# Optimization experiments

Hardware: AMD Instinct MI355X
Metric: run time of the kernel (lower is better)

Reference implementation:

```python
import jax, jax.numpy as jnp
import numpy as np

NB, T, NS, NC = 1024, 128, 12, 4
N = NS + NC  # stacked state+control dim


def setup_inputs() -> dict:
    key = jax.random.key(0)
    ks = jax.random.split(key, 7)
    x_init = jax.random.normal(ks[0], (NB, NS), jnp.float32)
    current_x = jax.random.normal(ks[1], (NB, T, NS), jnp.float32)
    current_u = jax.random.normal(ks[2], (NB, T, NC), jnp.float32)
    # symmetric positive-definite cost Hessian per (batch, t)
    G = 0.1 * jax.random.normal(ks[3], (NB, T, N, N), jnp.float32)
    Q = 0.5 * (G + jnp.swapaxes(G, -1, -2)) + jnp.eye(N, dtype=jnp.float32)
    p = jax.random.normal(ks[4], (NB, T, N), jnp.float32)
    # stable per-step dynamics linearizations
    A = 0.95 * jnp.eye(NS, dtype=jnp.float32) + 0.02 * jax.random.normal(ks[5], (NB, T, NS, NS), jnp.float32)
    Bmat = 0.1 * jax.random.normal(ks[6], (NB, T, NS, NC), jnp.float32)
    time = jnp.arange(T, dtype=jnp.int32)
    return {"x_init": x_init, "current_x": current_x, "current_u": current_u,
            "Q": Q, "p": p, "A": A, "Bmat": Bmat, "time": time}


def _lqr_backward(Q, p, A, Bmat):
    # time-major for scan: (T, NB, ...)
    Qs = jnp.moveaxis(Q, 1, 0)
    ps = jnp.moveaxis(p, 1, 0)
    As = jnp.moveaxis(A, 1, 0)
    Bs = jnp.moveaxis(Bmat, 1, 0)
    nb = Q.shape[0]
    V0 = jnp.zeros((nb, NS, NS), Q.dtype)  # V=0 reproduces the t==T-1 branch
    v0 = jnp.zeros((nb, NS), Q.dtype)

    def step(carry, inp):
        V, v = carry
        Qt0, pt, At, Bt = inp
        F = jnp.concatenate([At, Bt], axis=-1)          # (nb, ns, n)
        FT = jnp.swapaxes(F, -1, -2)                    # (nb, n, ns)
        Qt = Qt0 + FT @ V @ F                           # (nb, n, n)
        qt = pt + jnp.einsum('bsn,bs->bn', F, v)        # F^T v
        Qxx, Qxu = Qt[..., :NS, :NS], Qt[..., :NS, NS:]
        Qux, Quu = Qt[..., NS:, :NS], Qt[..., NS:, NS:]
        qx, qu = qt[..., :NS], qt[..., NS:]
        Quu_inv = jnp.linalg.pinv(Quu)                  # (nb, nc, nc)
        Kt = -(Quu_inv @ Qux)                           # (nb, nc, ns)
        kt = -jnp.einsum('bij,bj->bi', Quu_inv, qu)     # (nb, nc)
        KtT = jnp.swapaxes(Kt, -1, -2)
        Vn = Qxx + Qxu @ Kt + KtT @ Qux + KtT @ Quu @ Kt
        vn = (qx + jnp.einsum('bij,bj->bi', Qxu, kt)
              + jnp.einsum('bij,bj->bi', KtT, qu)
              + jnp.einsum('bij,bj->bi', KtT @ Quu, kt))
        return (Vn, vn), (Kt, kt)

    _, (K, k) = jax.lax.scan(step, (V0, v0), (Qs, ps, As, Bs), reverse=True)
    return jnp.moveaxis(K, 0, 1), jnp.moveaxis(k, 0, 1)


def _lqr_forward(x_init, current_u, Q, p, A, Bmat, K, k):
    Ks = jnp.moveaxis(K, 1, 0)
    ks_ = jnp.moveaxis(k, 1, 0)
    As = jnp.moveaxis(A, 1, 0)
    Bs = jnp.moveaxis(Bmat, 1, 0)
    cus = jnp.moveaxis(current_u, 1, 0)
    Qs = jnp.moveaxis(Q, 1, 0)
    ps = jnp.moveaxis(p, 1, 0)
    nb = x_init.shape[0]
    cost0 = jnp.zeros((nb,), x_init.dtype)

    def step(carry, inp):
        xt, cost = carry
        Kt, kt, At, Bt, cut, Qt, pt = inp
        # NOTE: original module never updates delta_x (stays zero), so delta_u == k_t
        ut = cut + kt
        xut = jnp.concatenate([xt, ut], axis=-1)        # (nb, n)
        xnext = jnp.einsum('bij,bj->bi', At, xt) + jnp.einsum('bij,bj->bi', Bt, ut)
        cost = cost + 0.5 * jnp.einsum('bi,bij,bj->b', xut, Qt, xut) + jnp.sum(xut * pt, axis=-1)
        return (xnext, cost), (xt, ut)

    (_, cost), (xs, us) = jax.lax.scan(step, (x_init, cost0), (Ks, ks_, As, Bs, cus, Qs, ps))
    # xs holds x_0..x_{T-1}, matching return of x[..., 0:-1, :]
    return jnp.moveaxis(xs, 0, 1), jnp.moveaxis(us, 0, 1), cost


def reference(x_init, current_x, current_u, Q, p, A, Bmat, time):
    K, k = _lqr_backward(Q, p, A, Bmat)
    return _lqr_forward(x_init, current_u, Q, p, A, Bmat, K, k)
```

## Files before the change

kernel.cpp:

```cpp
#include <hip/hip_runtime.h>


#define NBQ 1024
#define TT  128

__device__ __forceinline__ float dotf4(float4 a, float4 b) {
  return a.x*b.x + a.y*b.y + a.z*b.z + a.w*b.w;
}
__device__ __forceinline__ float dpp_qx1(float x) {
  return __int_as_float(__builtin_amdgcn_mov_dpp(__float_as_int(x), 0xB1, 0xF, 0xF, true));
}
__device__ __forceinline__ float dpp_qx2(float x) {
  return __int_as_float(__builtin_amdgcn_mov_dpp(__float_as_int(x), 0x4E, 0xF, 0xF, true));
}
template<int Q> __device__ __forceinline__ float4 bcast4(float4 v) {
  float4 r;
  r.x = __int_as_float(__builtin_amdgcn_mov_dpp(__float_as_int(v.x), Q*0x55, 0xF, 0xF, true));
  r.y = __int_as_float(__builtin_amdgcn_mov_dpp(__float_as_int(v.y), Q*0x55, 0xF, 0xF, true));
  r.z = __int_as_float(__builtin_amdgcn_mov_dpp(__float_as_int(v.z), Q*0x55, 0xF, 0xF, true));
  r.w = __int_as_float(__builtin_amdgcn_mov_dpp(__float_as_int(v.w), Q*0x55, 0xF, 0xF, true));
  return r;
}

#define MKS(K, O, MY)  { float4 mk_ = bcast4<O>(MY);                           \
  qt4_.x += gk_[K]*mk_.x; qt4_.y += gk_[K]*mk_.y;                              \
  qt4_.z += gk_[K]*mk_.z; qt4_.w += gk_[K]*mk_.w; }

#define BW_BODY(T_, QV, PV, CV, P0,P1,P2, S0,S1,S2, FTC, FTN)                  \
{                                                                              \
  const int  t_   = (T_);                                                      \
  const long bt_  = b*TT + t_;                                                 \
  const long btL_ = b*TT + ((t_ >= 4) ? (t_ - 4) : 0);                         \
  float4 qN_ = *(const float4*)(Qg + btL_*256 + qoff);                         \
  const float* fpL_ = fBase + btL_*fMul + fOfs;                                \
  float fN0_ = fpL_[0], fN1_ = fpL_[fstr_], fN2_ = fpL_[2*fstr_];              \
  float  pN_ = pg[btL_*16 + j];                                                \
  float  cN_ = cug[btL_*4 + q4];                                               \
             \
  FTN[wix] = P0; FTN[wix+1] = P1; FTN[wix+2] = P2;                             \
   \
  const float4* fj4_ = (const float4*)(FTC + j*12);                            \
  float4 f0_=fj4_[0], f1_=fj4_[1], f2_=fj4_[2];                                \
  const float4* vrow_ = (const float4*)(Vs + (3*r + dmin)*12);                 \
  float4 mv0_=vrow_[0], mv1_=vrow_[1], mv2_=vrow_[2];                          \
  float4 mw_ = *(const float4*)(vvS + 4*dmin);                                 \
   \
  float m0_, m1_, m2_;                                                         \
  { float4 r0_=bcast4<0>(mv0_), r1_=bcast4<0>(mv1_), r2_=bcast4<0>(mv2_);      \
    m0_ = dotf4(r0_,f0_)+dotf4(r1_,f1_)+dotf4(r2_,f2_); }                      \
  { float4 r0_=bcast4<1>(mv0_), r1_=bcast4<1>(mv1_), r2_=bcast4<1>(mv2_);      \
    m1_ = dotf4(r0_,f0_)+dotf4(r1_,f1_)+dotf4(r2_,f2_); }                      \
  { float4 r0_=bcast4<2>(mv0_), r1_=bcast4<2>(mv1_), r2_=bcast4<2>(mv2_);      \
    m2_ = dotf4(r0_,f0_)+dotf4(r1_,f1_)+dotf4(r2_,f2_); }                      \
  msh[(3*r+0)*16 + j] = m0_;                                                   \
  msh[(3*r+1)*16 + j] = m1_;                                                   \
  msh[(3*r+2)*16 + j] = m2_;                                                   \
                \
  float qtv_;                                                                  \
  { float4 w0_=bcast4<0>(mw_), w1_=bcast4<1>(mw_), w2_=bcast4<2>(mw_);         \
    qtv_ = PV + dotf4(w0_,f0_)+dotf4(w1_,f1_)+dotf4(w2_,f2_); }                \
                    \
  float gk_[12] = {f0_.x,f0_.y,f0_.z,f0_.w, f1_.x,f1_.y,f1_.z,f1_.w,           \
                   f2_.x,f2_.y,f2_.z,f2_.w};                                   \
  float4 mys0_ = *(const float4*)(msh + (3*q4+0)*16 + cb4);                    \
  float4 mys1_ = *(const float4*)(msh + (3*q4+1)*16 + cb4);                    \
  float4 mys2_ = *(const float4*)(msh + (3*q4+2)*16 + cb4);                    \
  float4 qt4_ = QV;                                                            \
  MKS(0,0,mys0_) MKS(1,0,mys1_) MKS(2,0,mys2_)                                 \
  MKS(3,1,mys0_) MKS(4,1,mys1_) MKS(5,1,mys2_)                                 \
  MKS(6,2,mys0_) MKS(7,2,mys1_) MKS(8,2,mys2_)                                 \
  MKS(9,3,mys0_) MKS(10,3,mys1_) MKS(11,3,mys2_)                               \
                                            \
  if (j >= 12)           *(float4*)(UxS + (j-12)*16 + cb4) = qt4_;             \
  if (cb == 3 && j < 12) *(float4*)(XuS + j*4) = qt4_;                         \
  if (l >= 12 && l < 16) quS[l-12] = qtv_;                                     \
   \
   \
  float4 mmA_ = *(const float4*)(UxS + 0*16 + 12);                             \
  float4 mmB_ = *(const float4*)(UxS + 1*16 + 12);                             \
  float4 mmC_ = *(const float4*)(UxS + 2*16 + 12);                             \
  float4 mmD_ = *(const float4*)(UxS + 3*16 + 12);                             \
  float4 ux0_ = *(const float4*)(UxS + 0*16 + cb4);                            \
  float4 ux1_ = *(const float4*)(UxS + 1*16 + cb4);                            \
  float4 ux2_ = *(const float4*)(UxS + 2*16 + cb4);                            \
  float4 ux3_ = *(const float4*)(UxS + 3*16 + cb4);                            \
  float4 quv_   = *(const float4*)quS;                                         \
  float4 xr_    = *(const float4*)(XuS + jc*4);                                \
  float mm_[16] = { mmA_.x, mmA_.y, mmA_.z, mmA_.w,                            \
                    mmB_.x, mmB_.y, mmB_.z, mmB_.w,                            \
                    mmC_.x, mmC_.y, mmC_.z, mmC_.w,                            \
                    mmD_.x, mmD_.y, mmD_.z, mmD_.w };                          \
    \
  float rdp_ = __builtin_amdgcn_rcpf(mm_[0]*mm_[5] - mm_[1]*mm_[1]);           \
  float pi00_ = mm_[5]*rdp_, pi01_ = -mm_[1]*rdp_, pi11_ = mm_[0]*rdp_;        \
  float w00_ = pi00_*mm_[2] + pi01_*mm_[6];                                    \
  float w01_ = pi00_*mm_[3] + pi01_*mm_[7];                                    \
  float w10_ = pi01_*mm_[2] + pi11_*mm_[6];                                    \
  float w11_ = pi01_*mm_[3] + pi11_*mm_[7];                                    \
  float t00_ = mm_[10] - (mm_[2]*w00_ + mm_[6]*w10_);                          \
  float t01_ = mm_[11] - (mm_[2]*w01_ + mm_[6]*w11_);                          \
  float t11_ = mm_[15] - (mm_[3]*w01_ + mm_[7]*w11_);                          \
  float rdt_ = __builtin_amdgcn_rcpf(t00_*t11_ - t01_*t01_);                   \
  float ti00_ = t11_*rdt_, ti01_ = -t01_*rdt_, ti11_ = t00_*rdt_;              \
  float u00_ = -(w00_*ti00_ + w01_*ti01_);                                     \
  float u01_ = -(w00_*ti01_ + w01_*ti11_);                                     \
  float u10_ = -(w10_*ti00_ + w11_*ti01_);                                     \
  float u11_ = -(w10_*ti01_ + w11_*ti11_);                                     \
  float i00_ = pi00_ - (u00_*w00_ + u01_*w01_);                                \
  float i01_ = pi01_ - (u00_*w10_ + u01_*w11_);                                \
  float i11_ = pi11_ - (u10_*w10_ + u11_*w11_);                                \
  float inv_[16] = { i00_, i01_, u00_, u01_,                                   \
                     i01_, i11_, u10_, u11_,                                   \
                     u00_, u10_, ti00_, ti01_,                                 \
                     u01_, u11_, ti01_, ti11_ };                               \
  float kt0_ = -(inv_[0] *quv_.x + inv_[1] *quv_.y + inv_[2] *quv_.z + inv_[3] *quv_.w); \
  float kt1_ = -(inv_[4] *quv_.x + inv_[5] *quv_.y + inv_[6] *quv_.z + inv_[7] *quv_.w); \
  float kt2_ = -(inv_[8] *quv_.x + inv_[9] *quv_.y + inv_[10]*quv_.z + inv_[11]*quv_.w); \
  float kt3_ = -(inv_[12]*quv_.x + inv_[13]*quv_.y + inv_[14]*quv_.z + inv_[15]*quv_.w); \
  float4 kc_[4];                                                               \
  _Pragma("unroll")                                                            \
  for (int c_ = 0; c_ < 4; ++c_) {                                             \
    kc_[c_].x = -(inv_[c_*4+0]*ux0_.x + inv_[c_*4+1]*ux1_.x + inv_[c_*4+2]*ux2_.x + inv_[c_*4+3]*ux3_.x); \
    kc_[c_].y = -(inv_[c_*4+0]*ux0_.y + inv_[c_*4+1]*ux1_.y + inv_[c_*4+2]*ux2_.y + inv_[c_*4+3]*ux3_.y); \
    kc_[c_].z = -(inv_[c_*4+0]*ux0_.z + inv_[c_*4+1]*ux1_.z + inv_[c_*4+2]*ux2_.z + inv_[c_*4+3]*ux3_.z); \
    kc_[c_].w = -(inv_[c_*4+0]*ux0_.w + inv_[c_*4+1]*ux1_.w + inv_[c_*4+2]*ux2_.w + inv_[c_*4+3]*ux3_.w); \
  }                                                                            \
  if (j < 12) {                                                                \
    float4 vn4_;                                                               \
    vn4_.x = qt4_.x + xr_.x*kc_[0].x + xr_.y*kc_[1].x + xr_.z*kc_[2].x + xr_.w*kc_[3].x; \
    vn4_.y = qt4_.y + xr_.x*kc_[0].y + xr_.y*kc_[1].y + xr_.z*kc_[2].y + xr_.w*kc_[3].y; \
    vn4_.z = qt4_.z + xr_.x*kc_[0].z + xr_.y*kc_[1].z + xr_.z*kc_[2].z + xr_.w*kc_[3].z; \
    vn4_.w = qt4_.w + xr_.x*kc_[0].w + xr_.y*kc_[1].w + xr_.z*kc_[2].w + xr_.w*kc_[3].w; \
    if (cb < 3) *(float4*)(Vs + j*12 + cb4) = vn4_;                            \
  }                                                                            \
  if (l < 12)                                                                  \
    vvS[l] = qtv_ + xr_.x*kt0_ + xr_.y*kt1_ + xr_.z*kt2_ + xr_.w*kt3_;         \
  float uv_ = CV + ((q4==0)?kt0_:(q4==1)?kt1_:(q4==2)?kt2_:kt3_);              \
  if (l < 4) { us_out[bt_*4 + l] = uv_; uL[t_*4 + l] = uv_; }                  \
  QV = qN_; S0 = fN0_; S1 = fN1_; S2 = fN2_; PV = pN_; CV = cN_;               \
}

__global__ __launch_bounds__(64, 1) void lqr_fused(
    const float* __restrict__ Qg, const float* __restrict__ pg,
    const float* __restrict__ Ag, const float* __restrict__ Bg,
    const float* __restrict__ cug, const float* __restrict__ xinit,
    float* __restrict__ out)
{
  __shared__ __align__(16) float lds[1376];
  float* FT0 = lds;
  float* FT1 = lds + 192;
  float* Vs  = lds + 384;
  float* vvS = lds + 528;
  float* msh = lds + 544;
  float* UxS = lds + 736;
  float* XuS = lds + 800;
  float* quS = lds + 848;
  float* uL  = lds + 864;

  const int l    = threadIdx.x;
  const int j    = l & 15;
  const int r    = l >> 4;
  const int q4   = l & 3;
  const int cb   = l >> 4;
  const int cb4  = cb << 2;
  const int dmin = (q4 < 2) ? q4 : 2;
  const int jc   = (j < 12) ? j : 11;
  const long b   = blockIdx.x;

  const int  n_   = l >> 2;
  const int  k0_  = 3*(l & 3);
  const int  wix  = n_*12 + k0_;
  const bool isA  = (n_ < 12);
  const float* fBase = isA ? Ag : Bg;
  const int  fMul  = isA ? 144 : 48;
  const int  fstr_ = isA ? 12  : 4;
  const int  fOfs  = isA ? (k0_*12 + n_) : (k0_*4 + (n_ - 12));
  const int  qoff  = j * 16 + cb4;

  float* xs_out = out;
  float* us_out = out + (long)NBQ*TT*12;
  float* c_out  = out + (long)NBQ*TT*12 + (long)NBQ*TT*4;

  if (j < 12 && cb < 3) *(float4*)(Vs + j*12 + cb4) = make_float4(0.f,0.f,0.f,0.f);
  if (l < 12) vvS[l] = 0.f;

  const long base = b*TT;
  float4 q3v,q2v,q1v,q0v;
  float  p3v,c3v,p2v,c2v,p1v,c1v,p0v,c0v;
  float  f3a,f3b,f3c, f2a,f2b,f2c, f1a,f1b,f1c, f0a,f0b,f0c;
  {
    long bt;
    bt = base+127; q3v=*(const float4*)(Qg+bt*256+qoff); p3v=pg[bt*16+j]; c3v=cug[bt*4+q4];
    { const float* fp = fBase + bt*fMul + fOfs; f3a=fp[0]; f3b=fp[fstr_]; f3c=fp[2*fstr_]; }
    bt = base+126; q2v=*(const float4*)(Qg+bt*256+qoff); p2v=pg[bt*16+j]; c2v=cug[bt*4+q4];
    { const float* fp = fBase + bt*fMul + fOfs; f2a=fp[0]; f2b=fp[fstr_]; f2c=fp[2*fstr_]; }
    bt = base+125; q1v=*(const float4*)(Qg+bt*256+qoff); p1v=pg[bt*16+j]; c1v=cug[bt*4+q4];
    { const float* fp = fBase + bt*fMul + fOfs; f1a=fp[0]; f1b=fp[fstr_]; f1c=fp[2*fstr_]; }
    bt = base+124; q0v=*(const float4*)(Qg+bt*256+qoff); p0v=pg[bt*16+j]; c0v=cug[bt*4+q4];
    { const float* fp = fBase + bt*fMul + fOfs; f0a=fp[0]; f0b=fp[fstr_]; f0c=fp[2*fstr_]; }
  }
  FT1[wix] = f3a; FT1[wix+1] = f3b; FT1[wix+2] = f3c;

  #pragma unroll 1
  for (int tb = TT-1; tb >= 3; tb -= 4) {
    BW_BODY(tb,   q3v, p3v, c3v,  f2a,f2b,f2c,  f3a,f3b,f3c, FT1, FT0)
    BW_BODY(tb-1, q2v, p2v, c2v,  f1a,f1b,f1c,  f2a,f2b,f2c, FT0, FT1)
    BW_BODY(tb-2, q1v, p1v, c1v,  f0a,f0b,f0c,  f1a,f1b,f1c, FT1, FT0)
    BW_BODY(tb-3, q0v, p0v, c0v,  f3a,f3b,f3c,  f0a,f0b,f0c, FT0, FT1)
  }

  const int i4  = l >> 2;
  const int c0f = q4 << 2;
  const int i4c = (i4 < 12) ? i4 : 11;
  const int sl0 = (c0f+0)<<2, sl1 = (c0f+1)<<2, sl2 = (c0f+2)<<2, sl3 = (c0f+3)<<2;
  float s = xinit[b*12 + i4c];
  float cacc = 0.f;

  const long bt0 = base;
  float4 qfA = *(const float4*)(Qg + bt0*256 + 4*l);
  float4 ffA = (q4 < 3) ? *(const float4*)(Ag + bt0*144 + i4c*12 + c0f)
                        : *(const float4*)(Bg + bt0*48  + i4c*4);
  float  pfA = pg[bt0*16 + i4];
  float4 qfB = *(const float4*)(Qg + (bt0+1)*256 + 4*l);
  float4 ffB = (q4 < 3) ? *(const float4*)(Ag + (bt0+1)*144 + i4c*12 + c0f)
                        : *(const float4*)(Bg + (bt0+1)*48  + i4c*4);
  float  pfB = pg[(bt0+1)*16 + i4];
  float4 qfC = *(const float4*)(Qg + (bt0+2)*256 + 4*l);
  float4 ffC = (q4 < 3) ? *(const float4*)(Ag + (bt0+2)*144 + i4c*12 + c0f)
                        : *(const float4*)(Bg + (bt0+2)*48  + i4c*4);
  float  pfC = pg[(bt0+2)*16 + i4];

  #pragma unroll 1
  for (int t = 0; t < TT; ++t) {
    const long btp = bt0 + ((t+3 < TT-1) ? t+3 : TT-1);
    float4 qfD = *(const float4*)(Qg + btp*256 + 4*l);
    float4 ffD = (q4 < 3) ? *(const float4*)(Ag + btp*144 + i4c*12 + c0f)
                          : *(const float4*)(Bg + btp*48  + i4c*4);
    float  pfD = pg[btp*16 + i4];

    float4 u4 = *(const float4*)(uL + t*4);

    float4 xg;
    xg.x = __shfl(s, sl0, 64); xg.y = __shfl(s, sl1, 64);
    xg.z = __shfl(s, sl2, 64); xg.w = __shfl(s, sl3, 64);
    float4 xuq = (q4 < 3) ? xg : u4;
    float xui = (i4 < 12) ? s
              : (i4 == 12) ? u4.x : (i4 == 13) ? u4.y : (i4 == 14) ? u4.z : u4.w;

    if (q4 == 0 && i4 < 12) xs_out[(bt0+t)*12 + i4] = s;

    cacc += 0.5f * xui * dotf4(qfA, xuq);
    if (q4 == 0) cacc += xui * pfA;

    float zx = dotf4(ffA, xuq);
    zx += dpp_qx1(zx);
    zx += dpp_qx2(zx);
    s = zx;

    qfA = qfB; ffA = ffB; pfA = pfB;
    qfB = qfC; ffB = ffC; pfB = pfC;
    qfC = qfD; ffC = ffD; pfC = pfD;
  }

  cacc += __shfl_xor(cacc, 32, 64);
  cacc += __shfl_xor(cacc, 16, 64);
  cacc += __shfl_xor(cacc, 8, 64);
  cacc += __shfl_xor(cacc, 4, 64);
  cacc += dpp_qx2(cacc);
  cacc += dpp_qx1(cacc);
  if (l == 0) c_out[b] = cacc;
}

extern "C" void kernel_launch(void* const* d_in, const int* in_sizes, int n_in,
                              void* d_out, int out_size, void* d_ws, size_t ws_size,
                              hipStream_t stream) {
  const float* xinit = (const float*)d_in[0];
  const float* cu = (const float*)d_in[2];
  const float* Q  = (const float*)d_in[3];
  const float* p  = (const float*)d_in[4];
  const float* A  = (const float*)d_in[5];
  const float* Bm = (const float*)d_in[6];
  float* out = (float*)d_out;

  lqr_fused<<<dim3(NBQ), dim3(64), 0, stream>>>(Q, p, A, Bm, cu, xinit, out);
}
```

Baseline: 381.8 us.

## Buffer per-step outputs in LDS, swizzle staging, and remove divergent branches

The per-timestep global stores of us and xs are now written into LDS buffers and flushed with coalesced 64-wide stores after each loop. The Qt staging area is unified into a swizzled float4 array, and the V/v state is stored per lane so stores need no branches. Divergent conditionals are replaced with dummy-slot pointer writes and a multiplicative mask. This aims to cut scattered global stores, LDS bank conflicts and branch overhead on the serial critical path, at the cost of more LDS per block.

```diff
diff --git a/kernel.cpp b/kernel.cpp
--- a/kernel.cpp
+++ b/kernel.cpp
@@ -3,6 +3,8 @@
 
 #define NBQ 1024
 #define TT  128
+
+#define SSLOT(x) ((x) ^ ((((x) >> 4) << 1)))
 
 __device__ __forceinline__ float dotf4(float4 a, float4 b) {
   return a.x*b.x + a.y*b.y + a.z*b.z + a.w*b.w;
@@ -29,7 +31,6 @@
 #define BW_BODY(T_, QV, PV, CV, P0,P1,P2, S0,S1,S2, FTC, FTN)                  \
 {                                                                              \
   const int  t_   = (T_);                                                      \
-  const long bt_  = b*TT + t_;                                                 \
   const long btL_ = b*TT + ((t_ >= 4) ? (t_ - 4) : 0);                         \
   float4 qN_ = *(const float4*)(Qg + btL_*256 + qoff);                         \
   const float* fpL_ = fBase + btL_*fMul + fOfs;                                \
@@ -38,12 +39,11 @@
   float  cN_ = cug[btL_*4 + q4];                                               \
              \
   FTN[wix] = P0; FTN[wix+1] = P1; FTN[wix+2] = P2;                             \
-   \
+          \
   const float4* fj4_ = (const float4*)(FTC + j*12);                            \
   float4 f0_=fj4_[0], f1_=fj4_[1], f2_=fj4_[2];                                \
-  const float4* vrow_ = (const float4*)(Vs + (3*r + dmin)*12);                 \
-  float4 mv0_=vrow_[0], mv1_=vrow_[1], mv2_=vrow_[2];                          \
-  float4 mw_ = *(const float4*)(vvS + 4*dmin);                                 \
+  float4 mv0_ = vns4[kR], mv1_ = vns4[16+kR], mv2_ = vns4[32+kR];              \
+  float4 mw_ = *(const float4*)(vvF + 4*dmin);                                 \
    \
   float m0_, m1_, m2_;                                                         \
   { float4 r0_=bcast4<0>(mv0_), r1_=bcast4<0>(mv1_), r2_=bcast4<0>(mv2_);      \
@@ -55,10 +55,11 @@
   msh[(3*r+0)*16 + j] = m0_;                                                   \
   msh[(3*r+1)*16 + j] = m1_;                                                   \
   msh[(3*r+2)*16 + j] = m2_;                                                   \
-                \
+   \
   float qtv_;                                                                  \
   { float4 w0_=bcast4<0>(mw_), w1_=bcast4<1>(mw_), w2_=bcast4<2>(mw_);         \
     qtv_ = PV + dotf4(w0_,f0_)+dotf4(w1_,f1_)+dotf4(w2_,f2_); }                \
+  qtS[l] = qtv_;                                                               \
                     \
   float gk_[12] = {f0_.x,f0_.y,f0_.z,f0_.w, f1_.x,f1_.y,f1_.z,f1_.w,           \
                    f2_.x,f2_.y,f2_.z,f2_.w};                                   \
@@ -70,27 +71,21 @@
   MKS(3,1,mys0_) MKS(4,1,mys1_) MKS(5,1,mys2_)                                 \
   MKS(6,2,mys0_) MKS(7,2,mys1_) MKS(8,2,mys2_)                                 \
   MKS(9,3,mys0_) MKS(10,3,mys1_) MKS(11,3,mys2_)                               \
-                                            \
-  if (j >= 12)           *(float4*)(UxS + (j-12)*16 + cb4) = qt4_;             \
-  if (cb == 3 && j < 12) *(float4*)(XuS + j*4) = qt4_;                         \
-  if (l >= 12 && l < 16) quS[l-12] = qtv_;                                     \
+              \
+  stg4[sw_] = qt4_;                                                            \
    \
-   \
-  float4 mmA_ = *(const float4*)(UxS + 0*16 + 12);                             \
-  float4 mmB_ = *(const float4*)(UxS + 1*16 + 12);                             \
-  float4 mmC_ = *(const float4*)(UxS + 2*16 + 12);                             \
-  float4 mmD_ = *(const float4*)(UxS + 3*16 + 12);                             \
-  float4 ux0_ = *(const float4*)(UxS + 0*16 + cb4);                            \
-  float4 ux1_ = *(const float4*)(UxS + 1*16 + cb4);                            \
-  float4 ux2_ = *(const float4*)(UxS + 2*16 + cb4);                            \
-  float4 ux3_ = *(const float4*)(UxS + 3*16 + cb4);                            \
-  float4 quv_   = *(const float4*)quS;                                         \
-  float4 xr_    = *(const float4*)(XuS + jc*4);                                \
+  float4 mmA_ = stg4[SSLOT(60)];                                               \
+  float4 mmB_ = stg4[SSLOT(61)];                                               \
+  float4 mmC_ = stg4[SSLOT(62)];                                               \
+  float4 mmD_ = stg4[SSLOT(63)];                                               \
+  float4 ux0_ = stg4[sux0], ux1_ = stg4[sux1], ux2_ = stg4[sux2], ux3_ = stg4[sux3]; \
+  float4 quv_ = *(const float4*)(qtS + 12);                                    \
+  float4 xr_  = stg4[sxr];                                                     \
   float mm_[16] = { mmA_.x, mmA_.y, mmA_.z, mmA_.w,                            \
                     mmB_.x, mmB_.y, mmB_.z, mmB_.w,                            \
                     mmC_.x, mmC_.y, mmC_.z, mmC_.w,                            \
                     mmD_.x, mmD_.y, mmD_.z, mmD_.w };                          \
-    \
+                           \
   float rdp_ = __builtin_amdgcn_rcpf(mm_[0]*mm_[5] - mm_[1]*mm_[1]);           \
   float pi00_ = mm_[5]*rdp_, pi01_ = -mm_[1]*rdp_, pi11_ = mm_[0]*rdp_;        \
   float w00_ = pi00_*mm_[2] + pi01_*mm_[6];                                    \
@@ -125,18 +120,16 @@
     kc_[c_].z = -(inv_[c_*4+0]*ux0_.z + inv_[c_*4+1]*ux1_.z + inv_[c_*4+2]*ux2_.z + inv_[c_*4+3]*ux3_.z); \
     kc_[c_].w = -(inv_[c_*4+0]*ux0_.w + inv_[c_*4+1]*ux1_.w + inv_[c_*4+2]*ux2_.w + inv_[c_*4+3]*ux3_.w); \
   }                                                                            \
-  if (j < 12) {                                                                \
-    float4 vn4_;                                                               \
-    vn4_.x = qt4_.x + xr_.x*kc_[0].x + xr_.y*kc_[1].x + xr_.z*kc_[2].x + xr_.w*kc_[3].x; \
-    vn4_.y = qt4_.y + xr_.x*kc_[0].y + xr_.y*kc_[1].y + xr_.z*kc_[2].y + xr_.w*kc_[3].y; \
-    vn4_.z = qt4_.z + xr_.x*kc_[0].z + xr_.y*kc_[1].z + xr_.z*kc_[2].z + xr_.w*kc_[3].z; \
-    vn4_.w = qt4_.w + xr_.x*kc_[0].w + xr_.y*kc_[1].w + xr_.z*kc_[2].w + xr_.w*kc_[3].w; \
-    if (cb < 3) *(float4*)(Vs + j*12 + cb4) = vn4_;                            \
-  }                                                                            \
-  if (l < 12)                                                                  \
-    vvS[l] = qtv_ + xr_.x*kt0_ + xr_.y*kt1_ + xr_.z*kt2_ + xr_.w*kt3_;         \
+                           \
+  float4 vn4_;                                                                 \
+  vn4_.x = qt4_.x + xr_.x*kc_[0].x + xr_.y*kc_[1].x + xr_.z*kc_[2].x + xr_.w*kc_[3].x; \
+  vn4_.y = qt4_.y + xr_.x*kc_[0].y + xr_.y*kc_[1].y + xr_.z*kc_[2].y + xr_.w*kc_[3].y; \
+  vn4_.z = qt4_.z + xr_.x*kc_[0].z + xr_.y*kc_[1].z + xr_.z*kc_[2].z + xr_.w*kc_[3].z; \
+  vn4_.w = qt4_.w + xr_.x*kc_[0].w + xr_.y*kc_[1].w + xr_.z*kc_[2].w + xr_.w*kc_[3].w; \
+  vns4[l] = vn4_;                                                              \
+  vvF[l] = qtv_ + xr_.x*kt0_ + xr_.y*kt1_ + xr_.z*kt2_ + xr_.w*kt3_;           \
   float uv_ = CV + ((q4==0)?kt0_:(q4==1)?kt1_:(q4==2)?kt2_:kt3_);              \
-  if (l < 4) { us_out[bt_*4 + l] = uv_; uL[t_*4 + l] = uv_; }                  \
+  upt[0] = uv_; upt -= ustp;                                                   \
   QV = qN_; S0 = fN0_; S1 = fN1_; S2 = fN2_; PV = pN_; CV = cN_;               \
 }
 
@@ -146,16 +139,17 @@
     const float* __restrict__ cug, const float* __restrict__ xinit,
     float* __restrict__ out)
 {
-  __shared__ __align__(16) float lds[1376];
-  float* FT0 = lds;
-  float* FT1 = lds + 192;
-  float* Vs  = lds + 384;
-  float* vvS = lds + 528;
-  float* msh = lds + 544;
-  float* UxS = lds + 736;
-  float* XuS = lds + 800;
-  float* quS = lds + 848;
-  float* uL  = lds + 864;
+  __shared__ __align__(16) float lds[3328];
+  float*  FT0  = lds;
+  float*  FT1  = lds + 192;
+  float*  msh  = lds + 384;
+  float4* stg4 = (float4*)(lds + 576);
+  float4* vns4 = (float4*)(lds + 832);
+  float*  qtS  = lds + 1088;
+  float*  vvF  = lds + 1152;
+  float*  uL   = lds + 1216;
+  float*  dmpS = lds + 1728;
+  float*  xsL  = lds + 1792;
 
   const int l    = threadIdx.x;
   const int j    = l & 15;
@@ -166,6 +160,12 @@
   const int dmin = (q4 < 2) ? q4 : 2;
   const int jc   = (j < 12) ? j : 11;
   const long b   = blockIdx.x;
+  const int  kR  = 3*r + dmin;
+
+  const int sw_  = SSLOT(l);
+  const int sux0 = SSLOT(16*cb + 12), sux1 = SSLOT(16*cb + 13);
+  const int sux2 = SSLOT(16*cb + 14), sux3 = SSLOT(16*cb + 15);
+  const int sxr  = SSLOT(48 + jc);
 
   const int  n_   = l >> 2;
   const int  k0_  = 3*(l & 3);
@@ -177,12 +177,16 @@
   const int  fOfs  = isA ? (k0_*12 + n_) : (k0_*4 + (n_ - 12));
   const int  qoff  = j * 16 + cb4;
 
+  float* up0 = (l < 4) ? (uL + l) : (dmpS + l);
+  const int ustp = (l < 4) ? 4 : 0;
+  float* upt = up0 + 127*ustp;
+
   float* xs_out = out;
   float* us_out = out + (long)NBQ*TT*12;
   float* c_out  = out + (long)NBQ*TT*12 + (long)NBQ*TT*4;
 
-  if (j < 12 && cb < 3) *(float4*)(Vs + j*12 + cb4) = make_float4(0.f,0.f,0.f,0.f);
-  if (l < 12) vvS[l] = 0.f;
+  vns4[l] = make_float4(0.f,0.f,0.f,0.f);
+  vvF[l]  = 0.f;
 
   const long base = b*TT;
   float4 q3v,q2v,q1v,q0v;
@@ -209,12 +213,20 @@
     BW_BODY(tb-3, q0v, p0v, c0v,  f3a,f3b,f3c,  f0a,f0b,f0c, FT0, FT1)
   }
 
+  #pragma unroll
+  for (int i_ = 0; i_ < 8; ++i_) us_out[b*512 + i_*64 + l] = uL[i_*64 + l];
+
   const int i4  = l >> 2;
   const int c0f = q4 << 2;
   const int i4c = (i4 < 12) ? i4 : 11;
   const int sl0 = (c0f+0)<<2, sl1 = (c0f+1)<<2, sl2 = (c0f+2)<<2, sl3 = (c0f+3)<<2;
   float s = xinit[b*12 + i4c];
   float cacc = 0.f;
+
+  const bool xc_ = (q4 == 0) && (i4 < 12);
+  float* xpt = xc_ ? (xsL + i4) : (dmpS + l);
+  const int xstp = xc_ ? 12 : 0;
+  const float q0m = (q4 == 0) ? 1.0f : 0.0f;
 
   const long bt0 = base;
   float4 qfA = *(const float4*)(Qg + bt0*256 + 4*l);
@@ -247,10 +259,10 @@
     float xui = (i4 < 12) ? s
               : (i4 == 12) ? u4.x : (i4 == 13) ? u4.y : (i4 == 14) ? u4.z : u4.w;
 
-    if (q4 == 0 && i4 < 12) xs_out[(bt0+t)*12 + i4] = s;
+    xpt[0] = s; xpt += xstp;
 
     cacc += 0.5f * xui * dotf4(qfA, xuq);
-    if (q4 == 0) cacc += xui * pfA;
+    cacc += q0m * (xui * pfA);
 
     float zx = dotf4(ffA, xuq);
     zx += dpp_qx1(zx);
@@ -261,6 +273,9 @@
     qfB = qfC; ffB = ffC; pfB = pfC;
     qfC = qfD; ffC = ffD; pfC = pfD;
   }
+
+  #pragma unroll
+  for (int i_ = 0; i_ < 24; ++i_) xs_out[b*1536 + i_*64 + l] = xsL[i_*64 + l];
 
   cacc += __shfl_xor(cacc, 32, 64);
   cacc += __shfl_xor(cacc, 16, 64);
```

After: 371.2 us. 1.03x faster.
